# Kernel optimization log

Measured on AMD Instinct MI355X. Metric: run time of the kernel, lower is better.

The kernel has to match this reference:

```python
import jax, jax.numpy as jnp
import numpy as np

N_NODES = 50000


def gcn_conv(x, edge_index, W, b):
    # PyG GCNConv: add self-loops, symmetric normalization, then aggregate.
    n = x.shape[0]
    loop = jnp.arange(n, dtype=edge_index.dtype)
    src = jnp.concatenate([edge_index[0], loop])  # [E+N]
    dst = jnp.concatenate([edge_index[1], loop])  # [E+N]
    deg = jax.ops.segment_sum(jnp.ones_like(dst, dtype=x.dtype), dst, num_segments=n)
    dinv = jnp.where(deg > 0, jax.lax.rsqrt(deg), 0.0)
    norm = dinv[src] * dinv[dst]                  # [E+N]
    xw = x @ W                                     # [N, out]
    msg = xw[src] * norm[:, None]                  # [E+N, out]
    out = jax.ops.segment_sum(msg, dst, num_segments=n)
    return out + b


def setup_inputs() -> dict:
    key = jax.random.key(0)
    ks = jax.random.split(key, 8)
    n, e, d, h, c = N_NODES, 800000, 128, 128, 40
    x = jax.random.normal(ks[0], (n, d), dtype=jnp.float32)
    edge_index = jax.random.randint(ks[1], (2, e), 0, n, dtype=jnp.int64)
    s = 0.05
    W1 = jax.random.normal(ks[2], (d, h), dtype=jnp.float32) * s
    b1 = jnp.zeros((h,), dtype=jnp.float32)
    W2 = jax.random.normal(ks[3], (h, h), dtype=jnp.float32) * s
    b2 = jnp.zeros((h,), dtype=jnp.float32)
    W3 = jax.random.normal(ks[4], (h, c), dtype=jnp.float32) * s
    b3 = jnp.zeros((c,), dtype=jnp.float32)
    return {"x": x, "edge_index": edge_index, "W1": W1, "b1": b1,
            "W2": W2, "b2": b2, "W3": W3, "b3": b3}


def reference(x, edge_index, W1, b1, W2, b2, W3, b3):
    # Block 0: GCNConv -> relu -> (dropout: identity in eval) -> residual
    h = jax.nn.relu(gcn_conv(x, edge_index, W1, b1)) + x
    # Block 1: GCNConv -> relu -> (dropout: identity in eval) -> residual
    h = jax.nn.relu(gcn_conv(h, edge_index, W2, b2)) + h
    # Final conv + log_softmax over classes
    out = gcn_conv(h, edge_index, W3, b3)
    return jax.nn.log_softmax(out, axis=1)
```

## Files before the change

### kernel.cpp

```cpp
#include <hip/hip_runtime.h>
#include <math.h>


#define HD 128
#define NC 40

typedef __attribute__((ext_vector_type(8))) short bfrag;
typedef __attribute__((ext_vector_type(4))) float facc;

__device__ __forceinline__ unsigned short f2bf(float f) {
  unsigned int u = __float_as_uint(f);
  u += 0x7FFFu + ((u >> 16) & 1u);
  return (unsigned short)(u >> 16);
}
__device__ __forceinline__ unsigned int packbf2(float a, float b) {
  return (unsigned int)f2bf(a) | ((unsigned int)f2bf(b) << 16);
}
__device__ __forceinline__ float2 bf2f2(unsigned int v) {
  float2 r;
  r.x = __uint_as_float(v << 16);
  r.y = __uint_as_float(v & 0xFFFF0000u);
  return r;
}
__device__ __forceinline__ float db(unsigned int u, int i) {
  return (float)(signed char)((u >> (8 * i)) & 0xFFu);
}

#define NCOPY 8


__global__ void k_init(int* __restrict__ cnt8, int* __restrict__ gtotal, int n8) {
  int i = blockIdx.x * 256 + threadIdx.x;
  if (i < n8) cnt8[i] = 0;
  if (i == 0) *gtotal = 0;
}

__global__ __launch_bounds__(256) void k_count_rank(
    const int* __restrict__ dst, int* __restrict__ cnt8,
    int* __restrict__ rank, int E, int n) {
  int e = blockIdx.x * 256 + threadIdx.x;
  if (e < E) {
    int copy = blockIdx.x & (NCOPY - 1);
    rank[e] = atomicAdd(&cnt8[copy * n + dst[e]], 1);
  }
}

__global__ __launch_bounds__(256) void k_alloc(
    const int* __restrict__ cnt8, int* __restrict__ row_start,
    int* __restrict__ row_end, int2* __restrict__ cinfo,
    float* __restrict__ dinv, int* __restrict__ gtotal, int n) {
  __shared__ int sh[256];
  __shared__ int base_sh;
  const int tid = threadIdx.x;
  int i = blockIdx.x * 256 + tid;
  int c[NCOPY];
  int v = 0;
  if (i < n) {
#pragma unroll
    for (int j = 0; j < NCOPY; ++j) {
      c[j] = cnt8[j * n + i];
      v += c[j];
    }
  }
  sh[tid] = v;
  __syncthreads();
  for (int off = 1; off < 256; off <<= 1) {
    int t = (tid >= off) ? sh[tid - off] : 0;
    __syncthreads();
    sh[tid] += t;
    __syncthreads();
  }
  if (tid == 255) base_sh = atomicAdd(gtotal, sh[255]);
  __syncthreads();
  if (i < n) {
    int start = base_sh + sh[tid] - v;
    float dv = rsqrtf((float)(v + 1));
    row_start[i] = start;
    row_end[i] = start + v;
    dinv[i] = dv;
    int base = start;
#pragma unroll
    for (int j = 0; j < NCOPY; ++j) {
      cinfo[(size_t)j * n + i] = make_int2(base, __float_as_int(dv));
      base += c[j];
    }
  }
}

__global__ __launch_bounds__(256) void k_fill(
    const int* __restrict__ src, const int* __restrict__ dst,
    const int* __restrict__ rank, const int2* __restrict__ cinfo,
    const float* __restrict__ dinv, int2* __restrict__ csr2, int E, int n) {
  int e = blockIdx.x * 256 + threadIdx.x;
  if (e < E) {
    int d = dst[e];
    int s = src[e];
    int r = rank[e];
    int copy = (e >> 8) & (NCOPY - 1);
    int2 ni = cinfo[(size_t)copy * n + d];
    float norm = dinv[s] * __int_as_float(ni.y);
    csr2[ni.x + r] = make_int2(s, __float_as_int(norm));
  }
}


__global__ __launch_bounds__(256) void k_wprep(
    const float* __restrict__ W1, const float* __restrict__ W2,
    unsigned short* __restrict__ W1t, unsigned short* __restrict__ W2t) {
  const float* W = blockIdx.x ? W2 : W1;
  unsigned short* Wt = blockIdx.x ? W2t : W1t;
  __shared__ unsigned short sh[HD * 136];
#pragma unroll
  for (int i = 0; i < 16; ++i) {
    int f4 = i * 256 + threadIdx.x;
    int r = f4 >> 5;
    int c = (f4 & 31) * 4;
    float4 v = *(const float4*)(W + r * HD + c);
    sh[(c + 0) * 136 + r] = f2bf(v.x);
    sh[(c + 1) * 136 + r] = f2bf(v.y);
    sh[(c + 2) * 136 + r] = f2bf(v.z);
    sh[(c + 3) * 136 + r] = f2bf(v.w);
  }
  __syncthreads();
#pragma unroll
  for (int i = 0; i < 8; ++i) {
    int g = i * 256 + threadIdx.x;
    int nrow = g >> 4, k16 = g & 15;
    uint4 v = *(const uint4*)(&sh[nrow * 136 + k16 * 8]);
    *(uint4*)(Wt + (size_t)g * 8) = v;
  }
}

__global__ __launch_bounds__(256) void k_wprep3(
    const float* __restrict__ W3, unsigned short* __restrict__ W3t) {
  __shared__ unsigned short sh[48 * 136];
  for (int i = threadIdx.x; i < 48 * 136; i += 256) sh[i] = 0;
  __syncthreads();
#pragma unroll
  for (int i = 0; i < 5; ++i) {
    int f4 = i * 256 + threadIdx.x;
    if (f4 < 1280) {
      int r = f4 / 10;
      int c = (f4 % 10) * 4;
      float4 v = *(const float4*)(W3 + r * NC + c);
      sh[(c + 0) * 136 + r] = f2bf(v.x);
      sh[(c + 1) * 136 + r] = f2bf(v.y);
      sh[(c + 2) * 136 + r] = f2bf(v.z);
      sh[(c + 3) * 136 + r] = f2bf(v.w);
    }
  }
  __syncthreads();
#pragma unroll
  for (int i = 0; i < 3; ++i) {
    int g = i * 256 + threadIdx.x;
    int nrow = g >> 4, k16 = g & 15;
    uint4 v = *(const uint4*)(&sh[nrow * 136 + k16 * 8]);
    *(uint4*)(W3t + (size_t)g * 8) = v;
  }
}


template <bool A_IS_F32>
__global__ __launch_bounds__(256) void gemm_mfma_f128(
    const float* __restrict__ Af, const unsigned short* __restrict__ Ab,
    const unsigned short* __restrict__ Wt,
    signed char* __restrict__ xw8, float* __restrict__ xscale, int n) {
  __shared__ unsigned short shWt[HD * 136];
  {
#pragma unroll
    for (int i = 0; i < 8; ++i) {
      int g = i * 256 + threadIdx.x;
      int nrow = g >> 4, k16 = g & 15;
      uint4 v = *(const uint4*)(Wt + (size_t)g * 8);
      *(uint4*)(&shWt[nrow * 136 + k16 * 8]) = v;
    }
  }

  const int lane = threadIdx.x & 63;
  const int w = threadIdx.x >> 6;
  const int m = blockIdx.x * 64 + w * 16 + (lane & 15);
  const int mc = min(m, n - 1);
  const int kbase = (lane >> 4) * 8;

  bfrag af[4];
  if constexpr (A_IS_F32) {
    const float* ap = Af + (size_t)mc * HD + kbase;
#pragma unroll
    for (int kk = 0; kk < 4; ++kk) {
      float4 lo = *(const float4*)(ap + kk * 32);
      float4 hi = *(const float4*)(ap + kk * 32 + 4);
      bfrag a;
      a[0] = (short)f2bf(lo.x); a[1] = (short)f2bf(lo.y);
      a[2] = (short)f2bf(lo.z); a[3] = (short)f2bf(lo.w);
      a[4] = (short)f2bf(hi.x); a[5] = (short)f2bf(hi.y);
      a[6] = (short)f2bf(hi.z); a[7] = (short)f2bf(hi.w);
      af[kk] = a;
    }
  } else {
    const unsigned short* ap = Ab + (size_t)mc * HD + kbase;
#pragma unroll
    for (int kk = 0; kk < 4; ++kk) af[kk] = *(const bfrag*)(ap + kk * 32);
  }

  __syncthreads();

  facc acc[8];
#pragma unroll
  for (int c = 0; c < 8; ++c) {
    acc[c][0] = 0.f; acc[c][1] = 0.f; acc[c][2] = 0.f; acc[c][3] = 0.f;
  }

#pragma unroll
  for (int kk = 0; kk < 4; ++kk) {
#pragma unroll
    for (int c = 0; c < 8; ++c) {
      bfrag bf = *(const bfrag*)(&shWt[(c * 16 + (lane & 15)) * 136 + kk * 32 + kbase]);
      acc[c] = __builtin_amdgcn_mfma_f32_16x16x32_bf16(af[kk], bf, acc[c], 0, 0, 0);
    }
  }

  float rmax[4];
#pragma unroll
  for (int q = 0; q < 4; ++q) {
    float mx = 0.f;
#pragma unroll
    for (int c = 0; c < 8; ++c) mx = fmaxf(mx, fabsf(acc[c][q]));
    rmax[q] = mx;
  }
#pragma unroll
  for (int off = 1; off < 16; off <<= 1) {
#pragma unroll
    for (int q = 0; q < 4; ++q) rmax[q] = fmaxf(rmax[q], __shfl_xor(rmax[q], off, 64));
  }

  const int rbase = blockIdx.x * 64 + w * 16 + (lane >> 4) * 4;
  const int col = lane & 15;
#pragma unroll
  for (int q = 0; q < 4; ++q) {
    int r = rbase + q;
    if (r < n) {
      float inv = (rmax[q] > 0.f) ? (127.f / rmax[q]) : 0.f;
      if (col == q) xscale[r] = rmax[q] * (1.f / 127.f);
#pragma unroll
      for (int c = 0; c < 8; ++c) {
        int v = __float2int_rn(acc[c][q] * inv);
        xw8[(size_t)r * HD + c * 16 + col] = (signed char)v;
      }
    }
  }
}


__global__ __launch_bounds__(256) void gemm_mfma_f40(
    const unsigned short* __restrict__ Ab,
    const unsigned short* __restrict__ Wt,
    unsigned short* __restrict__ out, int n) {
  __shared__ unsigned short shWt[48 * 136];
  {
#pragma unroll
    for (int i = 0; i < 3; ++i) {
      int g = i * 256 + threadIdx.x;
      int nrow = g >> 4, k16 = g & 15;
      uint4 v = *(const uint4*)(Wt + (size_t)g * 8);
      *(uint4*)(&shWt[nrow * 136 + k16 * 8]) = v;
    }
  }

  const int lane = threadIdx.x & 63;
  const int w = threadIdx.x >> 6;
  const int m = blockIdx.x * 64 + w * 16 + (lane & 15);
  const int mc = min(m, n - 1);
  const int kbase = (lane >> 4) * 8;

  bfrag af[4];
  const unsigned short* ap = Ab + (size_t)mc * HD + kbase;
#pragma unroll
  for (int kk = 0; kk < 4; ++kk) af[kk] = *(const bfrag*)(ap + kk * 32);

  __syncthreads();

  facc acc[3];
#pragma unroll
  for (int c = 0; c < 3; ++c) {
    acc[c][0] = 0.f; acc[c][1] = 0.f; acc[c][2] = 0.f; acc[c][3] = 0.f;
  }
#pragma unroll
  for (int kk = 0; kk < 4; ++kk) {
#pragma unroll
    for (int c = 0; c < 3; ++c) {
      bfrag bf = *(const bfrag*)(&shWt[(c * 16 + (lane & 15)) * 136 + kk * 32 + kbase]);
      acc[c] = __builtin_amdgcn_mfma_f32_16x16x32_bf16(af[kk], bf, acc[c], 0, 0, 0);
    }
  }

  const int rbase = blockIdx.x * 64 + w * 16 + (lane >> 4) * 4;
  const int col = lane & 15;
#pragma unroll
  for (int c = 0; c < 3; ++c) {
    int j = c * 16 + col;
    if (j < NC) {
#pragma unroll
      for (int q = 0; q < 4; ++q) {
        int r = rbase + q;
        if (r < n) out[(size_t)r * NC + j] = f2bf(acc[c][q]);
      }
    }
  }
}


__global__ __launch_bounds__(256) void agg_f128(
    const signed char* __restrict__ xw8, const float* __restrict__ xscale,
    const float* __restrict__ resid, const float* __restrict__ bias,
    const float* __restrict__ dinv,
    const int* __restrict__ row_start, const int* __restrict__ row_end,
    const int2* __restrict__ csr2, float* __restrict__ out,
    unsigned short* __restrict__ hb, int n) {
  const int node = (blockIdx.x * 256 + threadIdx.x) >> 4;
  if (node >= n) return;
  const int li = threadIdx.x & 15;
  const int f0 = li * 8;

  float di = dinv[node];
  float4 b01 = *(const float4*)(bias + f0);
  float4 b23 = *(const float4*)(bias + f0 + 4);
  uint2 su = *(const uint2*)(xw8 + (size_t)node * HD + f0);
  float ssc = xscale[node] * di * di;
  float a0 = fmaf(db(su.x, 0), ssc, b01.x);
  float a1 = fmaf(db(su.x, 1), ssc, b01.y);
  float a2 = fmaf(db(su.x, 2), ssc, b01.z);
  float a3 = fmaf(db(su.x, 3), ssc, b01.w);
  float a4 = fmaf(db(su.y, 0), ssc, b23.x);
  float a5 = fmaf(db(su.y, 1), ssc, b23.y);
  float a6 = fmaf(db(su.y, 2), ssc, b23.z);
  float a7 = fmaf(db(su.y, 3), ssc, b23.w);

  int k = row_start[node];
  const int end = row_end[node];
  for (; k + 4 <= end; k += 4) {
    int2 c0 = csr2[k], c1 = csr2[k + 1], c2 = csr2[k + 2], c3 = csr2[k + 3];
    uint2 u0 = *(const uint2*)(xw8 + (size_t)c0.x * HD + f0);
    uint2 u1 = *(const uint2*)(xw8 + (size_t)c1.x * HD + f0);
    uint2 u2 = *(const uint2*)(xw8 + (size_t)c2.x * HD + f0);
    uint2 u3 = *(const uint2*)(xw8 + (size_t)c3.x * HD + f0);
    float w0 = __int_as_float(c0.y) * xscale[c0.x];
    float w1 = __int_as_float(c1.y) * xscale[c1.x];
    float w2 = __int_as_float(c2.y) * xscale[c2.x];
    float w3 = __int_as_float(c3.y) * xscale[c3.x];
    a0 = fmaf(db(u0.x, 0), w0, a0); a1 = fmaf(db(u0.x, 1), w0, a1);
    a2 = fmaf(db(u0.x, 2), w0, a2); a3 = fmaf(db(u0.x, 3), w0, a3);
    a4 = fmaf(db(u0.y, 0), w0, a4); a5 = fmaf(db(u0.y, 1), w0, a5);
    a6 = fmaf(db(u0.y, 2), w0, a6); a7 = fmaf(db(u0.y, 3), w0, a7);
    a0 = fmaf(db(u1.x, 0), w1, a0); a1 = fmaf(db(u1.x, 1), w1, a1);
    a2 = fmaf(db(u1.x, 2), w1, a2); a3 = fmaf(db(u1.x, 3), w1, a3);
    a4 = fmaf(db(u1.y, 0), w1, a4); a5 = fmaf(db(u1.y, 1), w1, a5);
    a6 = fmaf(db(u1.y, 2), w1, a6); a7 = fmaf(db(u1.y, 3), w1, a7);
    a0 = fmaf(db(u2.x, 0), w2, a0); a1 = fmaf(db(u2.x, 1), w2, a1);
    a2 = fmaf(db(u2.x, 2), w2, a2); a3 = fmaf(db(u2.x, 3), w2, a3);
    a4 = fmaf(db(u2.y, 0), w2, a4); a5 = fmaf(db(u2.y, 1), w2, a5);
    a6 = fmaf(db(u2.y, 2), w2, a6); a7 = fmaf(db(u2.y, 3), w2, a7);
    a0 = fmaf(db(u3.x, 0), w3, a0); a1 = fmaf(db(u3.x, 1), w3, a1);
    a2 = fmaf(db(u3.x, 2), w3, a2); a3 = fmaf(db(u3.x, 3), w3, a3);
    a4 = fmaf(db(u3.y, 0), w3, a4); a5 = fmaf(db(u3.y, 1), w3, a5);
    a6 = fmaf(db(u3.y, 2), w3, a6); a7 = fmaf(db(u3.y, 3), w3, a7);
  }
  for (; k < end; ++k) {
    int2 c = csr2[k];
    uint2 u = *(const uint2*)(xw8 + (size_t)c.x * HD + f0);
    float w = __int_as_float(c.y) * xscale[c.x];
    a0 = fmaf(db(u.x, 0), w, a0); a1 = fmaf(db(u.x, 1), w, a1);
    a2 = fmaf(db(u.x, 2), w, a2); a3 = fmaf(db(u.x, 3), w, a3);
    a4 = fmaf(db(u.y, 0), w, a4); a5 = fmaf(db(u.y, 1), w, a5);
    a6 = fmaf(db(u.y, 2), w, a6); a7 = fmaf(db(u.y, 3), w, a7);
  }

  float4 r0 = *(const float4*)(resid + (size_t)node * HD + f0);
  float4 r1 = *(const float4*)(resid + (size_t)node * HD + f0 + 4);
  float4 o0, o1;
  o0.x = fmaxf(a0, 0.f) + r0.x; o0.y = fmaxf(a1, 0.f) + r0.y;
  o0.z = fmaxf(a2, 0.f) + r0.z; o0.w = fmaxf(a3, 0.f) + r0.w;
  o1.x = fmaxf(a4, 0.f) + r1.x; o1.y = fmaxf(a5, 0.f) + r1.y;
  o1.z = fmaxf(a6, 0.f) + r1.z; o1.w = fmaxf(a7, 0.f) + r1.w;
  if (out) {
    *(float4*)(out + (size_t)node * HD + f0) = o0;
    *(float4*)(out + (size_t)node * HD + f0 + 4) = o1;
  }
  if (hb) {
    uint4 hv;
    hv.x = packbf2(o0.x, o0.y);
    hv.y = packbf2(o0.z, o0.w);
    hv.z = packbf2(o1.x, o1.y);
    hv.w = packbf2(o1.z, o1.w);
    *(uint4*)(hb + (size_t)node * HD + f0) = hv;
  }
}


__global__ __launch_bounds__(256) void agg_f40_lsm(
    const unsigned short* __restrict__ xw, const float* __restrict__ dinv,
    const int* __restrict__ row_start, const int* __restrict__ row_end,
    const int2* __restrict__ csr2, const float* __restrict__ bias,
    float* __restrict__ out, int n) {
  const int node = (blockIdx.x * 256 + threadIdx.x) >> 4;
  if (node >= n) return;
  const int li = threadIdx.x & 15;
  const bool act = li < 10;
  const int f0 = li * 4;

  float a0 = 0.f, a1 = 0.f, a2 = 0.f, a3 = 0.f;
  float di = dinv[node];
  if (act) {
    float4 bv = *(const float4*)(bias + f0);
    uint2 su = *(const uint2*)(xw + (size_t)node * NC + f0);
    float2 s0 = bf2f2(su.x), s1 = bf2f2(su.y);
    float ssc = di * di;
    a0 = fmaf(s0.x, ssc, bv.x);
    a1 = fmaf(s0.y, ssc, bv.y);
    a2 = fmaf(s1.x, ssc, bv.z);
    a3 = fmaf(s1.y, ssc, bv.w);
  }

  int k = row_start[node];
  const int end = row_end[node];
  for (; k + 4 <= end; k += 4) {
    int2 c0 = csr2[k], c1 = csr2[k + 1], c2 = csr2[k + 2], c3 = csr2[k + 3];
    if (act) {
      uint2 u0 = *(const uint2*)(xw + (size_t)c0.x * NC + f0);
      uint2 u1 = *(const uint2*)(xw + (size_t)c1.x * NC + f0);
      uint2 u2 = *(const uint2*)(xw + (size_t)c2.x * NC + f0);
      uint2 u3 = *(const uint2*)(xw + (size_t)c3.x * NC + f0);
      float w0 = __int_as_float(c0.y), w1 = __int_as_float(c1.y);
      float w2 = __int_as_float(c2.y), w3 = __int_as_float(c3.y);
      float2 p, q;
      p = bf2f2(u0.x); q = bf2f2(u0.y);
      a0 = fmaf(p.x, w0, a0); a1 = fmaf(p.y, w0, a1);
      a2 = fmaf(q.x, w0, a2); a3 = fmaf(q.y, w0, a3);
      p = bf2f2(u1.x); q = bf2f2(u1.y);
      a0 = fmaf(p.x, w1, a0); a1 = fmaf(p.y, w1, a1);
      a2 = fmaf(q.x, w1, a2); a3 = fmaf(q.y, w1, a3);
      p = bf2f2(u2.x); q = bf2f2(u2.y);
      a0 = fmaf(p.x, w2, a0); a1 = fmaf(p.y, w2, a1);
      a2 = fmaf(q.x, w2, a2); a3 = fmaf(q.y, w2, a3);
      p = bf2f2(u3.x); q = bf2f2(u3.y);
      a0 = fmaf(p.x, w3, a0); a1 = fmaf(p.y, w3, a1);
      a2 = fmaf(q.x, w3, a2); a3 = fmaf(q.y, w3, a3);
    }
  }
  for (; k < end; ++k) {
    int2 c = csr2[k];
    if (act) {
      uint2 u = *(const uint2*)(xw + (size_t)c.x * NC + f0);
      float w = __int_as_float(c.y);
      float2 p = bf2f2(u.x), q = bf2f2(u.y);
      a0 = fmaf(p.x, w, a0); a1 = fmaf(p.y, w, a1);
      a2 = fmaf(q.x, w, a2); a3 = fmaf(q.y, w, a3);
    }
  }

  float m = act ? fmaxf(fmaxf(a0, a1), fmaxf(a2, a3)) : -3.0e38f;
  m = fmaxf(m, __shfl_xor(m, 1, 64));
  m = fmaxf(m, __shfl_xor(m, 2, 64));
  m = fmaxf(m, __shfl_xor(m, 4, 64));
  m = fmaxf(m, __shfl_xor(m, 8, 64));
  float s = act ? (expf(a0 - m) + expf(a1 - m) + expf(a2 - m) + expf(a3 - m)) : 0.f;
  s += __shfl_xor(s, 1, 64);
  s += __shfl_xor(s, 2, 64);
  s += __shfl_xor(s, 4, 64);
  s += __shfl_xor(s, 8, 64);
  if (act) {
    float lse = m + logf(s);
    float4 o;
    o.x = a0 - lse; o.y = a1 - lse; o.z = a2 - lse; o.w = a3 - lse;
    *(float4*)(out + (size_t)node * NC + f0) = o;
  }
}


extern "C" void kernel_launch(void* const* d_in, const int* in_sizes, int n_in,
                              void* d_out, int out_size, void* d_ws, size_t ws_size,
                              hipStream_t stream) {
  const float* x  = (const float*)d_in[0];
  const int*   ei = (const int*)d_in[1];
  const float* W1 = (const float*)d_in[2];
  const float* b1 = (const float*)d_in[3];
  const float* W2 = (const float*)d_in[4];
  const float* b2 = (const float*)d_in[5];
  const float* W3 = (const float*)d_in[6];
  const float* b3 = (const float*)d_in[7];
  float* out = (float*)d_out;

  const int n = in_sizes[0] / HD;
  const int E = in_sizes[1] / 2;
  const int* src = ei;
  const int* dst = ei + E;

  char* ws = (char*)d_ws;
  size_t off = 0;
  auto carve = [&](size_t bytes) -> void* {
    void* p = ws + off;
    off += (bytes + 255) & ~(size_t)255;
    return p;
  };
  int*   cnt8      = (int*)carve((size_t)n * NCOPY * 4);
  int*   row_start = (int*)carve((size_t)n * 4);
  int*   row_end   = (int*)carve((size_t)n * 4);
  float* dinv      = (float*)carve((size_t)n * 4);
  int2*  cinfo     = (int2*)carve((size_t)n * NCOPY * 8);
  int*   gtotal    = (int*)carve(256);
  unsigned short* w1t = (unsigned short*)carve((size_t)HD * HD * 2);
  unsigned short* w2t = (unsigned short*)carve((size_t)HD * HD * 2);
  unsigned short* w3t = (unsigned short*)carve((size_t)48 * HD * 2);
  int2*  csr2      = (int2*)carve((size_t)E * 8);
  signed char* xw8 = (signed char*)carve((size_t)n * HD);
  float* xscale    = (float*)carve((size_t)n * 4);
  unsigned short* xw40 = (unsigned short*)carve((size_t)n * NC * 2);
  unsigned short* hb  = (unsigned short*)carve((size_t)n * HD * 2);
  float* bufB      = (float*)carve((size_t)n * HD * 4);
  int*   rank      = (int*)bufB;

  const int gn8  = (n * NCOPY + 255) / 256;
  const int gE1  = (E + 255) / 256;
  const int gA   = (n + 15) / 16;
  const int gM   = (n + 63) / 64;

  k_init<<<gn8, 256, 0, stream>>>(cnt8, gtotal, n * NCOPY);
  k_wprep<<<2, 256, 0, stream>>>(W1, W2, w1t, w2t);
  k_wprep3<<<1, 256, 0, stream>>>(W3, w3t);
  k_count_rank<<<gE1, 256, 0, stream>>>(dst, cnt8, rank, E, n);
  k_alloc<<<(n + 255) / 256, 256, 0, stream>>>(cnt8, row_start, row_end, cinfo, dinv, gtotal, n);
  k_fill<<<gE1, 256, 0, stream>>>(src, dst, rank, cinfo, dinv, csr2, E, n);

  gemm_mfma_f128<true><<<gM, 256, 0, stream>>>(x, (const unsigned short*)nullptr, w1t, xw8, xscale, n);
  agg_f128<<<gA, 256, 0, stream>>>(xw8, xscale, x, b1, dinv, row_start, row_end, csr2, bufB, hb, n);

  gemm_mfma_f128<false><<<gM, 256, 0, stream>>>((const float*)nullptr, hb, w2t, xw8, xscale, n);
  agg_f128<<<gA, 256, 0, stream>>>(xw8, xscale, bufB, b2, dinv, row_start, row_end, csr2,
                                   (float*)nullptr, hb, n);

  gemm_mfma_f40<<<gM, 256, 0, stream>>>(hb, w3t, xw40, n);
  agg_f40_lsm<<<gA, 256, 0, stream>>>(xw40, dinv, row_start, row_end, csr2, b3, out, n);
}
```

Before: 168.2 us.

## Switch layer features from int8 to bf16, drop fp32 residual, fuse prep kernels

```diff
diff --git a/kernel.cpp b/kernel.cpp
--- a/kernel.cpp
+++ b/kernel.cpp
@@ -22,18 +22,70 @@
   r.y = __uint_as_float(v & 0xFFFF0000u);
   return r;
 }
-__device__ __forceinline__ float db(unsigned int u, int i) {
-  return (float)(signed char)((u >> (8 * i)) & 0xFFu);
-}
 
 #define NCOPY 8
 
 
-__global__ void k_init(int* __restrict__ cnt8, int* __restrict__ gtotal, int n8) {
-  int i = blockIdx.x * 256 + threadIdx.x;
-  if (i < n8) cnt8[i] = 0;
-  if (i == 0) *gtotal = 0;
-}
+__global__ __launch_bounds__(256) void k_prep(
+    const float* __restrict__ W1, const float* __restrict__ W2,
+    const float* __restrict__ W3,
+    unsigned short* __restrict__ W1t, unsigned short* __restrict__ W2t,
+    unsigned short* __restrict__ W3t,
+    int* __restrict__ cnt8, int* __restrict__ gtotal, int n8) {
+  __shared__ unsigned short sh[HD * 136];
+  if (blockIdx.x < 2) {
+    const float* W = blockIdx.x ? W2 : W1;
+    unsigned short* Wt = blockIdx.x ? W2t : W1t;
+#pragma unroll
+    for (int i = 0; i < 16; ++i) {
+      int f4 = i * 256 + threadIdx.x;
+      int r = f4 >> 5;
+      int c = (f4 & 31) * 4;
+      float4 v = *(const float4*)(W + r * HD + c);
+      sh[(c + 0) * 136 + r] = f2bf(v.x);
+      sh[(c + 1) * 136 + r] = f2bf(v.y);
+      sh[(c + 2) * 136 + r] = f2bf(v.z);
+      sh[(c + 3) * 136 + r] = f2bf(v.w);
+    }
+    __syncthreads();
+#pragma unroll
+    for (int i = 0; i < 8; ++i) {
+      int g = i * 256 + threadIdx.x;
+      int nrow = g >> 4, k16 = g & 15;
+      uint4 v = *(const uint4*)(&sh[nrow * 136 + k16 * 8]);
+      *(uint4*)(Wt + (size_t)g * 8) = v;
+    }
+  } else if (blockIdx.x == 2) {
+    for (int i = threadIdx.x; i < 48 * 136; i += 256) sh[i] = 0;
+    __syncthreads();
+#pragma unroll
+    for (int i = 0; i < 5; ++i) {
+      int f4 = i * 256 + threadIdx.x;
+      if (f4 < 1280) {
+        int r = f4 / 10;
+        int c = (f4 % 10) * 4;
+        float4 v = *(const float4*)(W3 + r * NC + c);
+        sh[(c + 0) * 136 + r] = f2bf(v.x);
+        sh[(c + 1) * 136 + r] = f2bf(v.y);
+        sh[(c + 2) * 136 + r] = f2bf(v.z);
+        sh[(c + 3) * 136 + r] = f2bf(v.w);
+      }
+    }
+    __syncthreads();
+#pragma unroll
+    for (int i = 0; i < 3; ++i) {
+      int g = i * 256 + threadIdx.x;
+      int nrow = g >> 4, k16 = g & 15;
+      uint4 v = *(const uint4*)(&sh[nrow * 136 + k16 * 8]);
+      *(uint4*)(W3t + (size_t)g * 8) = v;
+    }
+  } else {
+    int i = (blockIdx.x - 3) * 256 + threadIdx.x;
+    if (i < n8) cnt8[i] = 0;
+    if (i == 0) *gtotal = 0;
+  }
+}
+
 
 __global__ __launch_bounds__(256) void k_count_rank(
     const int* __restrict__ dst, int* __restrict__ cnt8,
@@ -104,67 +156,11 @@
 }
 
 
-__global__ __launch_bounds__(256) void k_wprep(
-    const float* __restrict__ W1, const float* __restrict__ W2,
-    unsigned short* __restrict__ W1t, unsigned short* __restrict__ W2t) {
-  const float* W = blockIdx.x ? W2 : W1;
-  unsigned short* Wt = blockIdx.x ? W2t : W1t;
-  __shared__ unsigned short sh[HD * 136];
-#pragma unroll
-  for (int i = 0; i < 16; ++i) {
-    int f4 = i * 256 + threadIdx.x;
-    int r = f4 >> 5;
-    int c = (f4 & 31) * 4;
-    float4 v = *(const float4*)(W + r * HD + c);
-    sh[(c + 0) * 136 + r] = f2bf(v.x);
-    sh[(c + 1) * 136 + r] = f2bf(v.y);
-    sh[(c + 2) * 136 + r] = f2bf(v.z);
-    sh[(c + 3) * 136 + r] = f2bf(v.w);
-  }
-  __syncthreads();
-#pragma unroll
-  for (int i = 0; i < 8; ++i) {
-    int g = i * 256 + threadIdx.x;
-    int nrow = g >> 4, k16 = g & 15;
-    uint4 v = *(const uint4*)(&sh[nrow * 136 + k16 * 8]);
-    *(uint4*)(Wt + (size_t)g * 8) = v;
-  }
-}
-
-__global__ __launch_bounds__(256) void k_wprep3(
-    const float* __restrict__ W3, unsigned short* __restrict__ W3t) {
-  __shared__ unsigned short sh[48 * 136];
-  for (int i = threadIdx.x; i < 48 * 136; i += 256) sh[i] = 0;
-  __syncthreads();
-#pragma unroll
-  for (int i = 0; i < 5; ++i) {
-    int f4 = i * 256 + threadIdx.x;
-    if (f4 < 1280) {
-      int r = f4 / 10;
-      int c = (f4 % 10) * 4;
-      float4 v = *(const float4*)(W3 + r * NC + c);
-      sh[(c + 0) * 136 + r] = f2bf(v.x);
-      sh[(c + 1) * 136 + r] = f2bf(v.y);
-      sh[(c + 2) * 136 + r] = f2bf(v.z);
-      sh[(c + 3) * 136 + r] = f2bf(v.w);
-    }
-  }
-  __syncthreads();
-#pragma unroll
-  for (int i = 0; i < 3; ++i) {
-    int g = i * 256 + threadIdx.x;
-    int nrow = g >> 4, k16 = g & 15;
-    uint4 v = *(const uint4*)(&sh[nrow * 136 + k16 * 8]);
-    *(uint4*)(W3t + (size_t)g * 8) = v;
-  }
-}
-
-
 template <bool A_IS_F32>
 __global__ __launch_bounds__(256) void gemm_mfma_f128(
     const float* __restrict__ Af, const unsigned short* __restrict__ Ab,
     const unsigned short* __restrict__ Wt,
-    signed char* __restrict__ xw8, float* __restrict__ xscale, int n) {
+    unsigned short* __restrict__ out, int n) {
   __shared__ unsigned short shWt[HD * 136];
   {
 #pragma unroll
@@ -219,33 +215,15 @@
     }
   }
 
-  float rmax[4];
-#pragma unroll
-  for (int q = 0; q < 4; ++q) {
-    float mx = 0.f;
-#pragma unroll
-    for (int c = 0; c < 8; ++c) mx = fmaxf(mx, fabsf(acc[c][q]));
-    rmax[q] = mx;
-  }
-#pragma unroll
-  for (int off = 1; off < 16; off <<= 1) {
-#pragma unroll
-    for (int q = 0; q < 4; ++q) rmax[q] = fmaxf(rmax[q], __shfl_xor(rmax[q], off, 64));
-  }
-
   const int rbase = blockIdx.x * 64 + w * 16 + (lane >> 4) * 4;
   const int col = lane & 15;
 #pragma unroll
   for (int q = 0; q < 4; ++q) {
     int r = rbase + q;
     if (r < n) {
-      float inv = (rmax[q] > 0.f) ? (127.f / rmax[q]) : 0.f;
-      if (col == q) xscale[r] = rmax[q] * (1.f / 127.f);
-#pragma unroll
-      for (int c = 0; c < 8; ++c) {
-        int v = __float2int_rn(acc[c][q] * inv);
-        xw8[(size_t)r * HD + c * 16 + col] = (signed char)v;
-      }
+#pragma unroll
+      for (int c = 0; c < 8; ++c)
+        out[(size_t)r * HD + c * 16 + col] = f2bf(acc[c][q]);
     }
   }
 }
@@ -309,13 +287,13 @@
 }
 
 
+template <bool RESID_F32>
 __global__ __launch_bounds__(256) void agg_f128(
-    const signed char* __restrict__ xw8, const float* __restrict__ xscale,
-    const float* __restrict__ resid, const float* __restrict__ bias,
-    const float* __restrict__ dinv,
+    const unsigned short* __restrict__ xw,
+    const float* __restrict__ residf, const unsigned short* __restrict__ residb,
+    const float* __restrict__ bias, const float* __restrict__ dinv,
     const int* __restrict__ row_start, const int* __restrict__ row_end,
-    const int2* __restrict__ csr2, float* __restrict__ out,
-    unsigned short* __restrict__ hb, int n) {
+    const int2* __restrict__ csr2, unsigned short* __restrict__ hbO, int n) {
   const int node = (blockIdx.x * 256 + threadIdx.x) >> 4;
   if (node >= n) return;
   const int li = threadIdx.x & 15;
@@ -324,75 +302,80 @@
   float di = dinv[node];
   float4 b01 = *(const float4*)(bias + f0);
   float4 b23 = *(const float4*)(bias + f0 + 4);
-  uint2 su = *(const uint2*)(xw8 + (size_t)node * HD + f0);
-  float ssc = xscale[node] * di * di;
-  float a0 = fmaf(db(su.x, 0), ssc, b01.x);
-  float a1 = fmaf(db(su.x, 1), ssc, b01.y);
-  float a2 = fmaf(db(su.x, 2), ssc, b01.z);
-  float a3 = fmaf(db(su.x, 3), ssc, b01.w);
-  float a4 = fmaf(db(su.y, 0), ssc, b23.x);
-  float a5 = fmaf(db(su.y, 1), ssc, b23.y);
-  float a6 = fmaf(db(su.y, 2), ssc, b23.z);
-  float a7 = fmaf(db(su.y, 3), ssc, b23.w);
+  uint4 su = *(const uint4*)(xw + (size_t)node * HD + f0);
+  float ssc = di * di;
+  float2 s0 = bf2f2(su.x), s1 = bf2f2(su.y), s2 = bf2f2(su.z), s3 = bf2f2(su.w);
+  float a0 = fmaf(s0.x, ssc, b01.x);
+  float a1 = fmaf(s0.y, ssc, b01.y);
+  float a2 = fmaf(s1.x, ssc, b01.z);
+  float a3 = fmaf(s1.y, ssc, b01.w);
+  float a4 = fmaf(s2.x, ssc, b23.x);
+  float a5 = fmaf(s2.y, ssc, b23.y);
+  float a6 = fmaf(s3.x, ssc, b23.z);
+  float a7 = fmaf(s3.y, ssc, b23.w);
 
   int k = row_start[node];
   const int end = row_end[node];
   for (; k + 4 <= end; k += 4) {
-    int2 c0 = csr2[k], c1 = csr2[k + 1], c2 = csr2[k + 2], c3 = csr2[k + 3];
-    uint2 u0 = *(const uint2*)(xw8 + (size_t)c0.x * HD + f0);
-    uint2 u1 = *(const uint2*)(xw8 + (size_t)c1.x * HD + f0);
-    uint2 u2 = *(const uint2*)(xw8 + (size_t)c2.x * HD + f0);
-    uint2 u3 = *(const uint2*)(xw8 + (size_t)c3.x * HD + f0);
-    float w0 = __int_as_float(c0.y) * xscale[c0.x];
-    float w1 = __int_as_float(c1.y) * xscale[c1.x];
-    float w2 = __int_as_float(c2.y) * xscale[c2.x];
-    float w3 = __int_as_float(c3.y) * xscale[c3.x];
-    a0 = fmaf(db(u0.x, 0), w0, a0); a1 = fmaf(db(u0.x, 1), w0, a1);
-    a2 = fmaf(db(u0.x, 2), w0, a2); a3 = fmaf(db(u0.x, 3), w0, a3);
-    a4 = fmaf(db(u0.y, 0), w0, a4); a5 = fmaf(db(u0.y, 1), w0, a5);
-    a6 = fmaf(db(u0.y, 2), w0, a6); a7 = fmaf(db(u0.y, 3), w0, a7);
-    a0 = fmaf(db(u1.x, 0), w1, a0); a1 = fmaf(db(u1.x, 1), w1, a1);
-    a2 = fmaf(db(u1.x, 2), w1, a2); a3 = fmaf(db(u1.x, 3), w1, a3);
-    a4 = fmaf(db(u1.y, 0), w1, a4); a5 = fmaf(db(u1.y, 1), w1, a5);
-    a6 = fmaf(db(u1.y, 2), w1, a6); a7 = fmaf(db(u1.y, 3), w1, a7);
-    a0 = fmaf(db(u2.x, 0), w2, a0); a1 = fmaf(db(u2.x, 1), w2, a1);
-    a2 = fmaf(db(u2.x, 2), w2, a2); a3 = fmaf(db(u2.x, 3), w2, a3);
-    a4 = fmaf(db(u2.y, 0), w2, a4); a5 = fmaf(db(u2.y, 1), w2, a5);
-    a6 = fmaf(db(u2.y, 2), w2, a6); a7 = fmaf(db(u2.y, 3), w2, a7);
-    a0 = fmaf(db(u3.x, 0), w3, a0); a1 = fmaf(db(u3.x, 1), w3, a1);
-    a2 = fmaf(db(u3.x, 2), w3, a2); a3 = fmaf(db(u3.x, 3), w3, a3);
-    a4 = fmaf(db(u3.y, 0), w3, a4); a5 = fmaf(db(u3.y, 1), w3, a5);
-    a6 = fmaf(db(u3.y, 2), w3, a6); a7 = fmaf(db(u3.y, 3), w3, a7);
+    int4 p01 = *(const int4*)(csr2 + k);
+    int4 p23 = *(const int4*)(csr2 + k + 2);
+    uint4 u0 = *(const uint4*)(xw + (size_t)p01.x * HD + f0);
+    uint4 u1 = *(const uint4*)(xw + (size_t)p01.z * HD + f0);
+    uint4 u2 = *(const uint4*)(xw + (size_t)p23.x * HD + f0);
+    uint4 u3 = *(const uint4*)(xw + (size_t)p23.z * HD + f0);
+    float w0 = __int_as_float(p01.y), w1 = __int_as_float(p01.w);
+    float w2 = __int_as_float(p23.y), w3 = __int_as_float(p23.w);
+    float2 v0, v1, v2, v3;
+    v0 = bf2f2(u0.x); v1 = bf2f2(u0.y); v2 = bf2f2(u0.z); v3 = bf2f2(u0.w);
+    a0 = fmaf(v0.x, w0, a0); a1 = fmaf(v0.y, w0, a1);
+    a2 = fmaf(v1.x, w0, a2); a3 = fmaf(v1.y, w0, a3);
+    a4 = fmaf(v2.x, w0, a4); a5 = fmaf(v2.y, w0, a5);
+    a6 = fmaf(v3.x, w0, a6); a7 = fmaf(v3.y, w0, a7);
+    v0 = bf2f2(u1.x); v1 = bf2f2(u1.y); v2 = bf2f2(u1.z); v3 = bf2f2(u1.w);
+    a0 = fmaf(v0.x, w1, a0); a1 = fmaf(v0.y, w1, a1);
+    a2 = fmaf(v1.x, w1, a2); a3 = fmaf(v1.y, w1, a3);
+    a4 = fmaf(v2.x, w1, a4); a5 = fmaf(v2.y, w1, a5);
+    a6 = fmaf(v3.x, w1, a6); a7 = fmaf(v3.y, w1, a7);
+    v0 = bf2f2(u2.x); v1 = bf2f2(u2.y); v2 = bf2f2(u2.z); v3 = bf2f2(u2.w);
+    a0 = fmaf(v0.x, w2, a0); a1 = fmaf(v0.y, w2, a1);
+    a2 = fmaf(v1.x, w2, a2); a3 = fmaf(v1.y, w2, a3);
+    a4 = fmaf(v2.x, w2, a4); a5 = fmaf(v2.y, w2, a5);
+    a6 = fmaf(v3.x, w2, a6); a7 = fmaf(v3.y, w2, a7);
+    v0 = bf2f2(u3.x); v1 = bf2f2(u3.y); v2 = bf2f2(u3.z); v3 = bf2f2(u3.w);
+    a0 = fmaf(v0.x, w3, a0); a1 = fmaf(v0.y, w3, a1);
+    a2 = fmaf(v1.x, w3, a2); a3 = fmaf(v1.y, w3, a3);
+    a4 = fmaf(v2.x, w3, a4); a5 = fmaf(v2.y, w3, a5);
+    a6 = fmaf(v3.x, w3, a6); a7 = fmaf(v3.y, w3, a7);
   }
   for (; k < end; ++k) {
     int2 c = csr2[k];
-    uint2 u = *(const uint2*)(xw8 + (size_t)c.x * HD + f0);
-    float w = __int_as_float(c.y) * xscale[c.x];
-    a0 = fmaf(db(u.x, 0), w, a0); a1 = fmaf(db(u.x, 1), w, a1);
-    a2 = fmaf(db(u.x, 2), w, a2); a3 = fmaf(db(u.x, 3), w, a3);
-    a4 = fmaf(db(u.y, 0), w, a4); a5 = fmaf(db(u.y, 1), w, a5);
-    a6 = fmaf(db(u.y, 2), w, a6); a7 = fmaf(db(u.y, 3), w, a7);
-  }
-
-  float4 r0 = *(const float4*)(resid + (size_t)node * HD + f0);
-  float4 r1 = *(const float4*)(resid + (size_t)node * HD + f0 + 4);
-  float4 o0, o1;
-  o0.x = fmaxf(a0, 0.f) + r0.x; o0.y = fmaxf(a1, 0.f) + r0.y;
-  o0.z = fmaxf(a2, 0.f) + r0.z; o0.w = fmaxf(a3, 0.f) + r0.w;
-  o1.x = fmaxf(a4, 0.f) + r1.x; o1.y = fmaxf(a5, 0.f) + r1.y;
-  o1.z = fmaxf(a6, 0.f) + r1.z; o1.w = fmaxf(a7, 0.f) + r1.w;
-  if (out) {
-    *(float4*)(out + (size_t)node * HD + f0) = o0;
-    *(float4*)(out + (size_t)node * HD + f0 + 4) = o1;
-  }
-  if (hb) {
-    uint4 hv;
-    hv.x = packbf2(o0.x, o0.y);
-    hv.y = packbf2(o0.z, o0.w);
-    hv.z = packbf2(o1.x, o1.y);
-    hv.w = packbf2(o1.z, o1.w);
-    *(uint4*)(hb + (size_t)node * HD + f0) = hv;
-  }
+    uint4 u = *(const uint4*)(xw + (size_t)c.x * HD + f0);
+    float wv = __int_as_float(c.y);
+    float2 v0 = bf2f2(u.x), v1 = bf2f2(u.y), v2 = bf2f2(u.z), v3 = bf2f2(u.w);
+    a0 = fmaf(v0.x, wv, a0); a1 = fmaf(v0.y, wv, a1);
+    a2 = fmaf(v1.x, wv, a2); a3 = fmaf(v1.y, wv, a3);
+    a4 = fmaf(v2.x, wv, a4); a5 = fmaf(v2.y, wv, a5);
+    a6 = fmaf(v3.x, wv, a6); a7 = fmaf(v3.y, wv, a7);
+  }
+
+  float r0, r1, r2, r3, r4, r5, r6, r7;
+  if constexpr (RESID_F32) {
+    float4 q0 = *(const float4*)(residf + (size_t)node * HD + f0);
+    float4 q1 = *(const float4*)(residf + (size_t)node * HD + f0 + 4);
+    r0 = q0.x; r1 = q0.y; r2 = q0.z; r3 = q0.w;
+    r4 = q1.x; r5 = q1.y; r6 = q1.z; r7 = q1.w;
+  } else {
+    uint4 q = *(const uint4*)(residb + (size_t)node * HD + f0);
+    float2 p0 = bf2f2(q.x), p1 = bf2f2(q.y), p2 = bf2f2(q.z), p3 = bf2f2(q.w);
+    r0 = p0.x; r1 = p0.y; r2 = p1.x; r3 = p1.y;
+    r4 = p2.x; r5 = p2.y; r6 = p3.x; r7 = p3.y;
+  }
+  uint4 hv;
+  hv.x = packbf2(fmaxf(a0, 0.f) + r0, fmaxf(a1, 0.f) + r1);
+  hv.y = packbf2(fmaxf(a2, 0.f) + r2, fmaxf(a3, 0.f) + r3);
+  hv.z = packbf2(fmaxf(a4, 0.f) + r4, fmaxf(a5, 0.f) + r5);
+  hv.w = packbf2(fmaxf(a6, 0.f) + r6, fmaxf(a7, 0.f) + r7);
+  *(uint4*)(hbO + (size_t)node * HD + f0) = hv;
 }
 
 
@@ -423,14 +406,15 @@
   int k = row_start[node];
   const int end = row_end[node];
   for (; k + 4 <= end; k += 4) {
-    int2 c0 = csr2[k], c1 = csr2[k + 1], c2 = csr2[k + 2], c3 = csr2[k + 3];
+    int4 p01 = *(const int4*)(csr2 + k);
+    int4 p23 = *(const int4*)(csr2 + k + 2);
     if (act) {
-      uint2 u0 = *(const uint2*)(xw + (size_t)c0.x * NC + f0);
-      uint2 u1 = *(const uint2*)(xw + (size_t)c1.x * NC + f0);
-      uint2 u2 = *(const uint2*)(xw + (size_t)c2.x * NC + f0);
-      uint2 u3 = *(const uint2*)(xw + (size_t)c3.x * NC + f0);
-      float w0 = __int_as_float(c0.y), w1 = __int_as_float(c1.y);
-      float w2 = __int_as_float(c2.y), w3 = __int_as_float(c3.y);
+      uint2 u0 = *(const uint2*)(xw + (size_t)p01.x * NC + f0);
+      uint2 u1 = *(const uint2*)(xw + (size_t)p01.z * NC + f0);
+      uint2 u2 = *(const uint2*)(xw + (size_t)p23.x * NC + f0);
+      uint2 u3 = *(const uint2*)(xw + (size_t)p23.z * NC + f0);
+      float w0 = __int_as_float(p01.y), w1 = __int_as_float(p01.w);
+      float w2 = __int_as_float(p23.y), w3 = __int_as_float(p23.w);
       float2 p, q;
       p = bf2f2(u0.x); q = bf2f2(u0.y);
       a0 = fmaf(p.x, w0, a0); a1 = fmaf(p.y, w0, a1);
@@ -511,32 +495,31 @@
   unsigned short* w2t = (unsigned short*)carve((size_t)HD * HD * 2);
   unsigned short* w3t = (unsigned short*)carve((size_t)48 * HD * 2);
   int2*  csr2      = (int2*)carve((size_t)E * 8);
-  signed char* xw8 = (signed char*)carve((size_t)n * HD);
-  float* xscale    = (float*)carve((size_t)n * 4);
+  unsigned short* xwb  = (unsigned short*)carve((size_t)n * HD * 2);
+  unsigned short* hb1  = (unsigned short*)carve((size_t)n * HD * 2);
+  unsigned short* hb2  = (unsigned short*)carve((size_t)n * HD * 2);
   unsigned short* xw40 = (unsigned short*)carve((size_t)n * NC * 2);
-  unsigned short* hb  = (unsigned short*)carve((size_t)n * HD * 2);
-  float* bufB      = (float*)carve((size_t)n * HD * 4);
-  int*   rank      = (int*)bufB;
+  int*   rank      = (int*)xwb;
 
   const int gn8  = (n * NCOPY + 255) / 256;
   const int gE1  = (E + 255) / 256;
   const int gA   = (n + 15) / 16;
   const int gM   = (n + 63) / 64;
 
-  k_init<<<gn8, 256, 0, stream>>>(cnt8, gtotal, n * NCOPY);
-  k_wprep<<<2, 256, 0, stream>>>(W1, W2, w1t, w2t);
-  k_wprep3<<<1, 256, 0, stream>>>(W3, w3t);
+  k_prep<<<gn8 + 3, 256, 0, stream>>>(W1, W2, W3, w1t, w2t, w3t, cnt8, gtotal,
+                                      n * NCOPY);
   k_count_rank<<<gE1, 256, 0, stream>>>(dst, cnt8, rank, E, n);
   k_alloc<<<(n + 255) / 256, 256, 0, stream>>>(cnt8, row_start, row_end, cinfo, dinv, gtotal, n);
   k_fill<<<gE1, 256, 0, stream>>>(src, dst, rank, cinfo, dinv, csr2, E, n);
 
-  gemm_mfma_f128<true><<<gM, 256, 0, stream>>>(x, (const unsigned short*)nullptr, w1t, xw8, xscale, n);
-  agg_f128<<<gA, 256, 0, stream>>>(xw8, xscale, x, b1, dinv, row_start, row_end, csr2, bufB, hb, n);
-
-  gemm_mfma_f128<false><<<gM, 256, 0, stream>>>((const float*)nullptr, hb, w2t, xw8, xscale, n);
-  agg_f128<<<gA, 256, 0, stream>>>(xw8, xscale, bufB, b2, dinv, row_start, row_end, csr2,
-                                   (float*)nullptr, hb, n);
-
-  gemm_mfma_f40<<<gM, 256, 0, stream>>>(hb, w3t, xw40, n);
+  gemm_mfma_f128<true><<<gM, 256, 0, stream>>>(x, (const unsigned short*)nullptr, w1t, xwb, n);
+  agg_f128<true><<<gA, 256, 0, stream>>>(xwb, x, (const unsigned short*)nullptr,
+                                         b1, dinv, row_start, row_end, csr2, hb1, n);
+
+  gemm_mfma_f128<false><<<gM, 256, 0, stream>>>((const float*)nullptr, hb1, w2t, xwb, n);
+  agg_f128<false><<<gA, 256, 0, stream>>>(xwb, (const float*)nullptr, hb1,
+                                          b2, dinv, row_start, row_end, csr2, hb2, n);
+
+  gemm_mfma_f40<<<gM, 256, 0, stream>>>(hb2, w3t, xw40, n);
   agg_f40_lsm<<<gA, 256, 0, stream>>>(xw40, dinv, row_start, row_end, csr2, b3, out, n);
 }
```

Result: slower. 173.2 us (+2.9%).
